# Kernel tuning notes

Hardware: AMD Instinct MI355X
Metric: run time of the kernel (lower is better)

## Reference

```python
import jax, jax.numpy as jnp
import numpy as np

B, N, M, D = 4, 1024, 1024, 64


def setup_inputs() -> dict:
    key = jax.random.key(0)
    k1, k2 = jax.random.split(key)
    lhs = jax.random.normal(k1, (B, N, D), dtype=jnp.float32)
    rhs = jax.random.normal(k2, (B, M, D), dtype=jnp.float32)
    return {"lhs": lhs, "rhs": rhs}


def reference(lhs, rhs):
    # SAD similarity: -sum_d |lhs[b,n,d] - rhs[b,m,d]|  -> [B, N, M]
    # Faithful to the torch module's broadcasted abs-diff reduction.
    diff = lhs[:, :, None, :] - rhs[:, None, :, :]  # [B, N, M, D]
    similarity = -jnp.abs(diff).sum(axis=-1)        # [B, N, M]
    return similarity
```

## Files before the change

kernel.cpp:

```cpp
#include <hip/hip_runtime.h>

#define BB 4
#define NN 1024
#define MM 1024
#define DD 64
#define TILE 64
#define PAD 68

__global__ __launch_bounds__(256, 4)
void SADSimilarity_38706245272206_kernel(const float* __restrict__ lhs,
                                         const float* __restrict__ rhs,
                                         float* __restrict__ out) {
    __shared__ float lt[TILE * PAD];
    __shared__ float rt[TILE * PAD];

    const int b  = blockIdx.z;
    const int n0 = blockIdx.y * TILE;
    const int m0 = blockIdx.x * TILE;
    const int tid = threadIdx.x;

    const float* lbase = lhs + (size_t)b * NN * DD + (size_t)n0 * DD;
    const float* rbase = rhs + (size_t)b * MM * DD + (size_t)m0 * DD;

    #pragma unroll
    for (int p = 0; p < 4; ++p) {
        int e   = tid + p * 256;
        int row = e >> 4;
        int q   = (e & 15) << 2;
        float4 lv = *(const float4*)(lbase + row * DD + q);
        float4 rv = *(const float4*)(rbase + row * DD + q);
        *(float4*)(&lt[row * PAD + q]) = lv;
        *(float4*)(&rt[row * PAD + q]) = rv;
    }
    __syncthreads();

    const int tx = tid & 15;
    const int ty = tid >> 4;

    float acc[4][4];
    #pragma unroll
    for (int i = 0; i < 4; ++i)
        #pragma unroll
        for (int j = 0; j < 4; ++j) acc[i][j] = 0.0f;

    #pragma unroll
    for (int dq = 0; dq < DD / 4; ++dq) {
        float4 l[4], r[4];
        #pragma unroll
        for (int i = 0; i < 4; ++i)
            l[i] = *(const float4*)(&lt[(ty + 16 * i) * PAD + dq * 4]);
        #pragma unroll
        for (int j = 0; j < 4; ++j)
            r[j] = *(const float4*)(&rt[(tx + 16 * j) * PAD + dq * 4]);
        #pragma unroll
        for (int i = 0; i < 4; ++i)
            #pragma unroll
            for (int j = 0; j < 4; ++j) {
                acc[i][j] += fabsf(l[i].x - r[j].x);
                acc[i][j] += fabsf(l[i].y - r[j].y);
                acc[i][j] += fabsf(l[i].z - r[j].z);
                acc[i][j] += fabsf(l[i].w - r[j].w);
            }
    }

    float* obase = out + (size_t)b * NN * MM + (size_t)n0 * MM + m0;
    #pragma unroll
    for (int i = 0; i < 4; ++i) {
        int row = ty + 16 * i;
        #pragma unroll
        for (int j = 0; j < 4; ++j) {
            obase[(size_t)row * MM + tx + 16 * j] = -acc[i][j];
        }
    }
}

extern "C" void kernel_launch(void* const* d_in, const int* in_sizes, int n_in,
                              void* d_out, int out_size, void* d_ws, size_t ws_size,
                              hipStream_t stream) {
    const float* lhs = (const float*)d_in[0];
    const float* rhs = (const float*)d_in[1];
    float* out = (float*)d_out;

    dim3 grid(MM / TILE, NN / TILE, BB);
    dim3 block(256, 1, 1);
    SADSimilarity_38706245272206_kernel<<<grid, block, 0, stream>>>(lhs, rhs, out);
}
```

Baseline: 70.22 us.

## Enlarge tiles to 128x128 with 8x8 per-thread outputs and double-buffered LDS reads

```diff
diff --git a/kernel.cpp b/kernel.cpp
--- a/kernel.cpp
+++ b/kernel.cpp
@@ -4,26 +4,40 @@
 #define NN 1024
 #define MM 1024
 #define DD 64
-#define TILE 64
+#define TN 128
+#define TM 128
 #define PAD 68
 
-__global__ __launch_bounds__(256, 4)
+
+#define COMPUTE(s)                                            \
+    _Pragma("unroll")                                         \
+    for (int i = 0; i < 8; ++i) {                             \
+        _Pragma("unroll")                                     \
+        for (int j = 0; j < 8; ++j) {                         \
+            acc[i][j] += fabsf(l[s][i].x - r[s][j].x);        \
+            acc[i][j] += fabsf(l[s][i].y - r[s][j].y);        \
+            acc[i][j] += fabsf(l[s][i].z - r[s][j].z);        \
+            acc[i][j] += fabsf(l[s][i].w - r[s][j].w);        \
+        }                                                     \
+    }
+
+__global__ __launch_bounds__(256, 1)
 void SADSimilarity_38706245272206_kernel(const float* __restrict__ lhs,
                                          const float* __restrict__ rhs,
                                          float* __restrict__ out) {
-    __shared__ float lt[TILE * PAD];
-    __shared__ float rt[TILE * PAD];
+    __shared__ float lt[TN * PAD];
+    __shared__ float rt[TM * PAD];
 
     const int b  = blockIdx.z;
-    const int n0 = blockIdx.y * TILE;
-    const int m0 = blockIdx.x * TILE;
+    const int n0 = blockIdx.y * TN;
+    const int m0 = blockIdx.x * TM;
     const int tid = threadIdx.x;
 
-    const float* lbase = lhs + (size_t)b * NN * DD + (size_t)n0 * DD;
-    const float* rbase = rhs + (size_t)b * MM * DD + (size_t)m0 * DD;
+    const float* lbase = lhs + ((size_t)b * NN + n0) * DD;
+    const float* rbase = rhs + ((size_t)b * MM + m0) * DD;
 
     #pragma unroll
-    for (int p = 0; p < 4; ++p) {
+    for (int p = 0; p < 8; ++p) {
         int e   = tid + p * 256;
         int row = e >> 4;
         int q   = (e & 15) << 2;
@@ -37,39 +51,45 @@
     const int tx = tid & 15;
     const int ty = tid >> 4;
 
-    float acc[4][4];
+    float acc[8][8];
     #pragma unroll
-    for (int i = 0; i < 4; ++i)
+    for (int i = 0; i < 8; ++i)
         #pragma unroll
-        for (int j = 0; j < 4; ++j) acc[i][j] = 0.0f;
+        for (int j = 0; j < 8; ++j) acc[i][j] = 0.0f;
+
+    float4 l[2][8], r[2][8];
 
     #pragma unroll
-    for (int dq = 0; dq < DD / 4; ++dq) {
-        float4 l[4], r[4];
+    for (int i = 0; i < 8; ++i) l[0][i] = *(const float4*)(&lt[(ty + 16 * i) * PAD]);
+    #pragma unroll
+    for (int j = 0; j < 8; ++j) r[0][j] = *(const float4*)(&rt[(tx + 16 * j) * PAD]);
+
+    for (int dq = 0; dq < DD / 4; dq += 2) {
+        const int o1 = (dq + 1) * 4;
+        const int o2 = ((dq + 2) & 15) * 4;
+
         #pragma unroll
-        for (int i = 0; i < 4; ++i)
-            l[i] = *(const float4*)(&lt[(ty + 16 * i) * PAD + dq * 4]);
+        for (int i = 0; i < 8; ++i) l[1][i] = *(const float4*)(&lt[(ty + 16 * i) * PAD + o1]);
         #pragma unroll
-        for (int j = 0; j < 4; ++j)
-            r[j] = *(const float4*)(&rt[(tx + 16 * j) * PAD + dq * 4]);
+        for (int j = 0; j < 8; ++j) r[1][j] = *(const float4*)(&rt[(tx + 16 * j) * PAD + o1]);
+
+        COMPUTE(0)
+
         #pragma unroll
-        for (int i = 0; i < 4; ++i)
-            #pragma unroll
-            for (int j = 0; j < 4; ++j) {
-                acc[i][j] += fabsf(l[i].x - r[j].x);
-                acc[i][j] += fabsf(l[i].y - r[j].y);
-                acc[i][j] += fabsf(l[i].z - r[j].z);
-                acc[i][j] += fabsf(l[i].w - r[j].w);
-            }
+        for (int i = 0; i < 8; ++i) l[0][i] = *(const float4*)(&lt[(ty + 16 * i) * PAD + o2]);
+        #pragma unroll
+        for (int j = 0; j < 8; ++j) r[0][j] = *(const float4*)(&rt[(tx + 16 * j) * PAD + o2]);
+
+        COMPUTE(1)
     }
 
-    float* obase = out + (size_t)b * NN * MM + (size_t)n0 * MM + m0;
+    float* obase = out + ((size_t)b * NN + n0) * MM + m0;
     #pragma unroll
-    for (int i = 0; i < 4; ++i) {
-        int row = ty + 16 * i;
+    for (int i = 0; i < 8; ++i) {
+        float* orow = obase + (size_t)(ty + 16 * i) * MM;
         #pragma unroll
-        for (int j = 0; j < 4; ++j) {
-            obase[(size_t)row * MM + tx + 16 * j] = -acc[i][j];
+        for (int j = 0; j < 8; ++j) {
+            orow[tx + 16 * j] = -acc[i][j];
         }
     }
 }
@@ -81,7 +101,7 @@
     const float* rhs = (const float*)d_in[1];
     float* out = (float*)d_out;
 
-    dim3 grid(MM / TILE, NN / TILE, BB);
+    dim3 grid(MM / TM, NN / TN, BB);
     dim3 block(256, 1, 1);
     SADSimilarity_38706245272206_kernel<<<grid, block, 0, stream>>>(lhs, rhs, out);
 }
```

Measured after the change: 82.36 us. 17.3% more time.
